# Kernel tuning notes

Hardware: AMD Instinct MI355X
Metric: run time of the kernel (lower is better)

Reference implementation:

```python
import jax, jax.numpy as jnp
import numpy as np

N = 65536          # flattened batch of latent vectors
D = 64             # latent_dim
K = 1024           # codebook_size


def setup_inputs() -> dict:
    key = jax.random.key(0)
    k1, k2 = jax.random.split(key)
    x = jax.random.normal(k1, (N, D), dtype=jnp.float32)
    # codebook init: uniform(-1/K, 1/K) as in the torch module
    W = jax.random.uniform(k2, (K, D), dtype=jnp.float32,
                           minval=-1.0 / K, maxval=1.0 / K)
    return {"x": x, "W": W}


def reference(x, W):
    L2 = jnp.sum(x * x, axis=1, keepdims=True)          # [N, 1]
    C2 = jnp.sum(W * W, axis=1)[None, :]                # [1, K]
    CL = x @ W.T                                        # [N, K]
    distances = L2 - 2.0 * CL + C2
    closest = jnp.argmin(distances, axis=-1)            # [N] int
    # gather nearest codebook vectors (equivalent to one-hot @ W)
    quantized = W[closest]                              # [N, D]
    return quantized, closest
```

## Files before the change

### kernel.cpp

```cpp
#include <hip/hip_runtime.h>
#include <math.h>

#define NROWS 65536
#define DDIM  64
#define KCB   1024

__global__ void vq_c2_kernel(const float* __restrict__ W, float* __restrict__ C2) {
    int j = blockIdx.x * blockDim.x + threadIdx.x;
    if (j >= KCB) return;
    const float* w = W + (size_t)j * DDIM;
    float r[8];
#pragma unroll
    for (int m = 0; m < 8; ++m) r[m] = __fmul_rn(w[m], w[m]);
#pragma unroll
    for (int i = 8; i < 64; i += 8) {
#pragma unroll
        for (int m = 0; m < 8; ++m)
            r[m] = __fadd_rn(r[m], __fmul_rn(w[i + m], w[i + m]));
    }
    float res = __fadd_rn(
        __fadd_rn(__fadd_rn(r[0], r[1]), __fadd_rn(r[2], r[3])),
        __fadd_rn(__fadd_rn(r[4], r[5]), __fadd_rn(r[6], r[7])));
    C2[j] = res;
}

__global__ void __launch_bounds__(256, 4)
vq_main_kernel(const float* __restrict__ x, const float* __restrict__ W,
               const float* __restrict__ C2, int* __restrict__ cls_i,
               float* __restrict__ cls_f) {
    __shared__ float s_bd[4][64];
    __shared__ int   s_bi[4][64];

    const int lane = threadIdx.x & 63;
    const int s    = __builtin_amdgcn_readfirstlane(threadIdx.x >> 6);
    const int row  = blockIdx.x * 64 + lane;

    const float* xr = x + (size_t)row * DDIM;
    float xv[64];
#pragma unroll
    for (int k = 0; k < 64; k += 4) {
        float4 v = *(const float4*)(xr + k);
        xv[k] = v.x; xv[k + 1] = v.y; xv[k + 2] = v.z; xv[k + 3] = v.w;
    }

    float r[8];
#pragma unroll
    for (int m = 0; m < 8; ++m) r[m] = __fmul_rn(xv[m], xv[m]);
#pragma unroll
    for (int i = 8; i < 64; i += 8) {
#pragma unroll
        for (int m = 0; m < 8; ++m)
            r[m] = __fadd_rn(r[m], __fmul_rn(xv[i + m], xv[i + m]));
    }
    const float L2 = __fadd_rn(
        __fadd_rn(__fadd_rn(r[0], r[1]), __fadd_rn(r[2], r[3])),
        __fadd_rn(__fadd_rn(r[4], r[5]), __fadd_rn(r[6], r[7])));

    float best = INFINITY;
    int   bidx = 0;
    const int j0 = s * 256;
    for (int jj = 0; jj < 256; ++jj) {
        const int j = j0 + jj;
        const float* wr = W + (size_t)j * DDIM;
        float acc = 0.0f;
#pragma unroll
        for (int k = 0; k < 64; ++k)
            acc = __builtin_fmaf(xv[k], wr[k], acc);
        const float dist = __fadd_rn(__fsub_rn(L2, __fmul_rn(2.0f, acc)), C2[j]);
        if (dist < best) { best = dist; bidx = j; }
    }

    s_bd[s][lane] = best;
    s_bi[s][lane] = bidx;
    __syncthreads();

    if (s == 0) {
        float b  = s_bd[0][lane];
        int   bi = s_bi[0][lane];
#pragma unroll
        for (int t = 1; t < 4; ++t) {
            const float d = s_bd[t][lane];
            if (d < b) { b = d; bi = s_bi[t][lane]; }
        }
        cls_i[row] = bi;
        cls_f[row] = (float)bi;
    }
}

__global__ void vq_gather_kernel(const float* __restrict__ W,
                                 const int* __restrict__ cls,
                                 float* __restrict__ outq) {
    const int t = blockIdx.x * blockDim.x + threadIdx.x;
    const int i = t >> 4;
    const int q = t & 15;
    const int j = cls[i];
    const float4 v = *(const float4*)(W + (size_t)j * DDIM + q * 4);
    *(float4*)(outq + (size_t)i * DDIM + q * 4) = v;
}

extern "C" void kernel_launch(void* const* d_in, const int* in_sizes, int n_in,
                              void* d_out, int out_size, void* d_ws, size_t ws_size,
                              hipStream_t stream) {
    const float* x = (const float*)d_in[0];
    const float* W = (const float*)d_in[1];

    float* outq = (float*)d_out;
    float* outi = (float*)d_out + (size_t)NROWS * DDIM;

    float* C2  = (float*)d_ws;
    int*   cls = (int*)((char*)d_ws + 4096);

    hipLaunchKernelGGL(vq_c2_kernel, dim3(KCB / 256), dim3(256), 0, stream, W, C2);
    hipLaunchKernelGGL(vq_main_kernel, dim3(NROWS / 64), dim3(256), 0, stream,
                       x, W, C2, cls, outi);
    hipLaunchKernelGGL(vq_gather_kernel, dim3((NROWS * 16) / 256), dim3(256), 0,
                       stream, W, cls, outq);
}
```

Measured before the change: 222.0 us.

## Fuse codebook gather into main kernel and unroll distance loop by two

The separate gather kernel is folded into the main argmin kernel: the chosen indices are staged in shared memory and the block copies the selected codebook rows to the output after a barrier. This drops one launch and the global round trip of the index array. The distance loop now handles two codewords per iteration, so each loaded x value is reused twice, and an empty asm keeps xv in registers. The costs are an extra block-wide barrier and higher register pressure from the two accumulators.

```diff
diff --git a/kernel.cpp b/kernel.cpp
--- a/kernel.cpp
+++ b/kernel.cpp
@@ -26,10 +26,11 @@
 
 __global__ void __launch_bounds__(256, 4)
 vq_main_kernel(const float* __restrict__ x, const float* __restrict__ W,
-               const float* __restrict__ C2, int* __restrict__ cls_i,
+               const float* __restrict__ C2, float* __restrict__ outq,
                float* __restrict__ cls_f) {
     __shared__ float s_bd[4][64];
     __shared__ int   s_bi[4][64];
+    __shared__ int   s_bj[64];
 
     const int lane = threadIdx.x & 63;
     const int s    = __builtin_amdgcn_readfirstlane(threadIdx.x >> 6);
@@ -59,15 +60,23 @@
     float best = INFINITY;
     int   bidx = 0;
     const int j0 = s * 256;
-    for (int jj = 0; jj < 256; ++jj) {
-        const int j = j0 + jj;
-        const float* wr = W + (size_t)j * DDIM;
-        float acc = 0.0f;
+    for (int jj = 0; jj < 256; jj += 2) {
 #pragma unroll
         for (int k = 0; k < 64; ++k)
-            acc = __builtin_fmaf(xv[k], wr[k], acc);
-        const float dist = __fadd_rn(__fsub_rn(L2, __fmul_rn(2.0f, acc)), C2[j]);
-        if (dist < best) { best = dist; bidx = j; }
+            asm volatile("" : "+v"(xv[k]));
+
+        const float* w0 = W + (size_t)(j0 + jj) * DDIM;
+        const float* w1 = w0 + DDIM;
+        float a0 = 0.0f, a1 = 0.0f;
+#pragma unroll
+        for (int k = 0; k < 64; ++k) {
+            a0 = __builtin_fmaf(xv[k], w0[k], a0);
+            a1 = __builtin_fmaf(xv[k], w1[k], a1);
+        }
+        const float d0 = __fadd_rn(__fsub_rn(L2, __fmul_rn(2.0f, a0)), C2[j0 + jj]);
+        const float d1 = __fadd_rn(__fsub_rn(L2, __fmul_rn(2.0f, a1)), C2[j0 + jj + 1]);
+        if (d0 < best) { best = d0; bidx = j0 + jj; }
+        if (d1 < best) { best = d1; bidx = j0 + jj + 1; }
     }
 
     s_bd[s][lane] = best;
@@ -82,20 +91,20 @@
             const float d = s_bd[t][lane];
             if (d < b) { b = d; bi = s_bi[t][lane]; }
         }
-        cls_i[row] = bi;
+        s_bj[lane] = bi;
         cls_f[row] = (float)bi;
     }
-}
+    __syncthreads();
 
-__global__ void vq_gather_kernel(const float* __restrict__ W,
-                                 const int* __restrict__ cls,
-                                 float* __restrict__ outq) {
-    const int t = blockIdx.x * blockDim.x + threadIdx.x;
-    const int i = t >> 4;
-    const int q = t & 15;
-    const int j = cls[i];
-    const float4 v = *(const float4*)(W + (size_t)j * DDIM + q * 4);
-    *(float4*)(outq + (size_t)i * DDIM + q * 4) = v;
+#pragma unroll
+    for (int m = 0; m < 4; ++m) {
+        const int chunk = (int)threadIdx.x + m * 256;
+        const int rr    = chunk >> 4;
+        const int q     = chunk & 15;
+        const int j     = s_bj[rr];
+        const float4 v  = *(const float4*)(W + (size_t)j * DDIM + q * 4);
+        *(float4*)(outq + ((size_t)blockIdx.x * 64 + rr) * DDIM + q * 4) = v;
+    }
 }
 
 extern "C" void kernel_launch(void* const* d_in, const int* in_sizes, int n_in,
@@ -107,12 +116,9 @@
     float* outq = (float*)d_out;
     float* outi = (float*)d_out + (size_t)NROWS * DDIM;
 
-    float* C2  = (float*)d_ws;
-    int*   cls = (int*)((char*)d_ws + 4096);
+    float* C2 = (float*)d_ws;
 
     hipLaunchKernelGGL(vq_c2_kernel, dim3(KCB / 256), dim3(256), 0, stream, W, C2);
     hipLaunchKernelGGL(vq_main_kernel, dim3(NROWS / 64), dim3(256), 0, stream,
-                       x, W, C2, cls, outi);
-    hipLaunchKernelGGL(vq_gather_kernel, dim3((NROWS * 16) / 256), dim3(256), 0,
-                       stream, W, cls, outq);
+                       x, W, C2, outq, outi);
 }
```

New measurement: 241.2 us. +8.6%, slower.

## Stage codebook tiles in per-wave LDS with register prefetch of next tile

Applied to the files above, without the earlier changes.

Each wave now copies 16-row tiles of its codebook slice from global memory into its own LDS buffer. It prefetches the next tile into registers while computing distances from LDS using broadcast float4 reads. Previously each row's weights were read straight from global memory, where wave-uniform addresses probably compiled to scalar loads. The change adds LDS traffic and relies on in-order LDS access within a wave rather than a barrier. The inner loop over tile rows is no longer unrolled.

```diff
diff --git a/kernel.cpp b/kernel.cpp
--- a/kernel.cpp
+++ b/kernel.cpp
@@ -4,6 +4,8 @@
 #define NROWS 65536
 #define DDIM  64
 #define KCB   1024
+#define TILE  16
+#define NTILE (256 / TILE)
 
 __global__ void vq_c2_kernel(const float* __restrict__ W, float* __restrict__ C2) {
     int j = blockIdx.x * blockDim.x + threadIdx.x;
@@ -28,8 +30,9 @@
 vq_main_kernel(const float* __restrict__ x, const float* __restrict__ W,
                const float* __restrict__ C2, int* __restrict__ cls_i,
                float* __restrict__ cls_f) {
-    __shared__ float s_bd[4][64];
-    __shared__ int   s_bi[4][64];
+    __shared__ float4 sW4[4][TILE * DDIM / 4];
+    __shared__ float  s_bd[4][64];
+    __shared__ int    s_bi[4][64];
 
     const int lane = threadIdx.x & 63;
     const int s    = __builtin_amdgcn_readfirstlane(threadIdx.x >> 6);
@@ -59,15 +62,41 @@
     float best = INFINITY;
     int   bidx = 0;
     const int j0 = s * 256;
-    for (int jj = 0; jj < 256; ++jj) {
-        const int j = j0 + jj;
-        const float* wr = W + (size_t)j * DDIM;
-        float acc = 0.0f;
+    const float4* wg = (const float4*)(W + (size_t)j0 * DDIM);
+
+    float4 stg[4];
 #pragma unroll
-        for (int k = 0; k < 64; ++k)
-            acc = __builtin_fmaf(xv[k], wr[k], acc);
-        const float dist = __fadd_rn(__fsub_rn(L2, __fmul_rn(2.0f, acc)), C2[j]);
-        if (dist < best) { best = dist; bidx = j; }
+    for (int q = 0; q < 4; ++q) stg[q] = wg[q * 64 + lane];
+
+#pragma unroll 1
+    for (int t = 0; t < NTILE; ++t) {
+        float4* buf = &sW4[s][0];
+#pragma unroll
+        for (int q = 0; q < 4; ++q) buf[q * 64 + lane] = stg[q];
+
+        if (t < NTILE - 1) {
+            const float4* wgn = wg + (t + 1) * 256;
+#pragma unroll
+            for (int q = 0; q < 4; ++q) stg[q] = wgn[q * 64 + lane];
+        }
+
+#pragma unroll 1
+        for (int jj = 0; jj < TILE; ++jj) {
+            const float4* wl = buf + jj * 16;
+            float acc = 0.0f;
+#pragma unroll
+            for (int c = 0; c < 16; ++c) {
+                const float4 wv = wl[c];
+                acc = __builtin_fmaf(xv[4 * c + 0], wv.x, acc);
+                acc = __builtin_fmaf(xv[4 * c + 1], wv.y, acc);
+                acc = __builtin_fmaf(xv[4 * c + 2], wv.z, acc);
+                acc = __builtin_fmaf(xv[4 * c + 3], wv.w, acc);
+            }
+            const int j = j0 + t * TILE + jj;
+            const float dist =
+                __fadd_rn(__fsub_rn(L2, __fmul_rn(2.0f, acc)), C2[j]);
+            if (dist < best) { best = dist; bidx = j; }
+        }
     }
 
     s_bd[s][lane] = best;
```

Result: slower. 252.4 us (+13.7%).
